# Kernel optimization log

Hardware: AMD Instinct MI355X
Metric: run time of the kernel (lower is better)

Reference implementation:

```python
import jax, jax.numpy as jnp
import numpy as np

N_HEADS = 4
D_HEAD = 32  # out_features // n_heads = 128 // 4
NEG_SLOPE = 0.2


def setup_inputs() -> dict:
    key = jax.random.key(0)
    k_x, k_adj, k_w, k_a = jax.random.split(key, 4)
    B, N, F_in, F_out = 4, 2048, 128, 128
    x = jax.random.normal(k_x, (B, N, F_in), dtype=jnp.float32)
    adj = jax.random.randint(k_adj, (B, N, N), 0, 2, dtype=jnp.int32)
    # Linear weight stored as [in, out] (torch stores [out, in]; math identical: x @ W)
    w_scale = np.sqrt(2.0 / (F_in + F_out))  # xavier-ish
    W = jax.random.normal(k_w, (F_in, F_out), dtype=jnp.float32) * w_scale
    a = jax.random.normal(k_a, (N_HEADS, 2 * D_HEAD), dtype=jnp.float32) * np.sqrt(2.0 / (2 * D_HEAD))
    return {"x": x, "adj": adj, "W": W, "a": a}


def reference(x, adj, W, a):
    B, N, _ = x.shape
    # project and split heads: [B, H, N, D]
    h = jnp.einsum('bnf,fo->bno', x, W).reshape(B, N, N_HEADS, D_HEAD).transpose(0, 2, 1, 3)
    # additive attention logits
    e_src = jnp.einsum('bhnd,hd->bhn', h, a[:, :D_HEAD])  # [B,H,N]
    e_dst = jnp.einsum('bhnd,hd->bhn', h, a[:, D_HEAD:])  # [B,H,N]
    e = e_src[:, :, :, None] + e_dst[:, :, None, :]       # [B,H,N,N]
    e = jnp.where(e > 0, e, NEG_SLOPE * e)                # leaky_relu(0.2)
    mask = (adj[:, None, :, :] == 0)                      # [B,1,N,N] -> broadcast over heads
    e = jnp.where(mask, -jnp.inf, e)
    alpha = jax.nn.softmax(e, axis=-1)                    # dropout omitted (eval mode)
    out = jnp.einsum('bhnm,bhmd->bhnd', alpha, h)         # weighted aggregation
    out = out.transpose(0, 2, 1, 3).reshape(B, N, N_HEADS * D_HEAD)
    return jax.nn.elu(out)
```

## Files before the change

kernel.cpp:

```cpp
#include <hip/hip_runtime.h>
#include <hip/hip_bf16.h>

#define BB 4
#define NN 2048
#define FIN 128
#define NH 4
#define DH 32
#define NS 0.2f

typedef unsigned int u32;
typedef unsigned short u16;
typedef unsigned long long u64;
typedef __attribute__((ext_vector_type(8))) short short8;
typedef __attribute__((ext_vector_type(4))) float f32x4;
typedef __attribute__((ext_vector_type(4))) unsigned int u32x4;

#define OFF_ES   0
#define OFF_PQ   32768
#define OFF_HT   65536
#define OFF_BITS 589824

__device__ __forceinline__ u16 f2bf_rne(float f) {
  unsigned u = __float_as_uint(f);
  return (u16)((u + 0x7fffu + ((u >> 16) & 1u)) >> 16);
}

__device__ __forceinline__ int bitmask(u32 w, int e) {
#if __has_builtin(__builtin_amdgcn_sbfe)
  return __builtin_amdgcn_sbfe((int)w, e, 1);
#else
  return ((int)(w << (31 - e))) >> 31;
#endif
}

__global__ __launch_bounds__(256) void k_pack(const int* __restrict__ adj,
                                              u32* __restrict__ bitsT) {
  __shared__ u32 tile[64][4];
  const int row0 = blockIdx.x * 4;
  const int wv = threadIdx.x >> 6;
  const int lane = threadIdx.x & 63;
  const int b = row0 >> 11, n0 = row0 & (NN - 1);
  const int* src = adj + (size_t)(row0 + wv) * NN;
#pragma unroll 8
  for (int it = 0; it < 32; ++it) {
    const u64 m = __ballot(src[it * 64 + lane] != 0);
    if (lane == 0) {
      tile[2 * it][wv] = (u32)m;
      tile[2 * it + 1][wv] = (u32)(m >> 32);
    }
  }
  __syncthreads();
  const int word = threadIdx.x >> 2, r = threadIdx.x & 3;
  bitsT[(size_t)b * 64 * NN + (size_t)word * NN + n0 + r] = tile[word][r];
}

__global__ __launch_bounds__(256) void k_proj(
    const float* __restrict__ x, const float* __restrict__ W,
    const float* __restrict__ a, u16* __restrict__ hT,
    float* __restrict__ e_src, u32* __restrict__ PQ) {
  __shared__ float Ws[FIN * 128];
  const int tid = threadIdx.x;
  const int f = tid & 127, g = tid >> 7;
  const float4* Wg4 = (const float4*)W;
  float4* Ws4 = (float4*)Ws;
#pragma unroll
  for (int t = 0; t < 16; ++t) Ws4[t * 256 + tid] = Wg4[t * 256 + tid];
  __syncthreads();

  const int rb = blockIdx.x * 16 + g * 8;
  const int head = f >> 5, d = f & 31;
  const int b = rb >> 11, n0 = rb & (NN - 1);
  const int bh = b * NH + head;
  const float a_s = a[head * (2 * DH) + d];
  const float a_d = a[head * (2 * DH) + DH + d];

  float acc[8];
#pragma unroll
  for (int r = 0; r < 8; ++r) acc[r] = 0.f;

  const float* xb = x + (size_t)rb * FIN;
  for (int k = 0; k < FIN; ++k) {
    const float wv = Ws[k * 128 + f];
#pragma unroll
    for (int r = 0; r < 8; ++r) acc[r] = fmaf(wv, xb[r * FIN + k], acc[r]);
  }

  u16 hs[8];
#pragma unroll
  for (int r = 0; r < 8; ++r) hs[r] = f2bf_rne(acc[r]);
  u16* dst = hT + ((size_t)bh * DH + d) * NN + n0;
  *(int4*)dst = *(int4*)&hs[0];

#pragma unroll
  for (int r = 0; r < 8; ++r) {
    float s1 = acc[r] * a_s;
    float s2 = acc[r] * a_d;
#pragma unroll
    for (int off = 16; off >= 1; off >>= 1) {
      s1 += __shfl_xor(s1, off);
      s2 += __shfl_xor(s2, off);
    }
    if (d == 0) {
      e_src[(size_t)bh * NN + n0 + r] = s1;
      const u32 pb = f2bf_rne(__expf(s2));
      const u32 qb = f2bf_rne(__expf(NS * s2));
      PQ[(size_t)bh * NN + n0 + r] = (qb << 16) | pb;
    }
  }
}

__global__ __launch_bounds__(256, 2) void k_attn(
    const u16* __restrict__ hT, const float* __restrict__ e_src,
    const u32* __restrict__ PQv, const u32* __restrict__ bitsT,
    float* __restrict__ out) {
  __shared__ float part[4][64][33];
  __shared__ float sp[4][4][16];

  const int bid = blockIdx.x;
  const int bh = bid >> 5;
  const int it = bid & 31;
  const int b = bh >> 2, head = bh & 3;

  const int w = threadIdx.x >> 6;
  const int lane = threadIdx.x & 63;
  const int lg = lane >> 4, lm = lane & 15;

  float A[4], B[4];
#pragma unroll
  for (int rs = 0; rs < 4; ++rs) {
    const float es = e_src[(size_t)bh * NN + it * 64 + rs * 16 + lm];
    A[rs] = __expf(es);
    B[rs] = __expf(NS * es);
  }

  const int jwbase = w * 512;
  const u32* PQb = PQv + (size_t)bh * NN + jwbase;
  const u16* hb0 = hT + ((size_t)bh * DH + lm) * NN + jwbase;
  const u16* hb1 = hT + ((size_t)bh * DH + 16 + lm) * NN + jwbase;
  const u32* btb = bitsT + (size_t)b * 64 * NN + (size_t)(w * 16) * NN + it * 64 + lm;
  const int shamt = lg * 8;
  const int jb = lg * 8;

  short8 ones;
#pragma unroll
  for (int e = 0; e < 8; ++e) ones[e] = (short)0x3F80;

  f32x4 acc00 = {0,0,0,0}, acc01 = {0,0,0,0};
  f32x4 acc10 = {0,0,0,0}, acc11 = {0,0,0,0};
  f32x4 acc20 = {0,0,0,0}, acc21 = {0,0,0,0};
  f32x4 acc30 = {0,0,0,0}, acc31 = {0,0,0,0};
  f32x4 accS0 = {0,0,0,0}, accS1 = {0,0,0,0};
  f32x4 accS2 = {0,0,0,0}, accS3 = {0,0,0,0};

#pragma unroll 4
  for (int t = 0; t < 16; ++t) {
    const int jj = t * 32 + jb;
    const u32x4 pqa = *(const u32x4*)(PQb + jj);
    const u32x4 pqb = *(const u32x4*)(PQb + jj + 4);
    const short8 hv0 = *(const short8*)(hb0 + jj);
    const short8 hv1 = *(const short8*)(hb1 + jj);
    const u32* btw = btb + (size_t)t * NN;
    const u32 wsh0 = btw[0] >> shamt;
    const u32 wsh1 = btw[16] >> shamt;
    const u32 wsh2 = btw[32] >> shamt;
    const u32 wsh3 = btw[48] >> shamt;
    short8 af0, af1, af2, af3;
#pragma unroll
    for (int e = 0; e < 8; ++e) {
      const u32 pq = (e < 4) ? pqa[e] : pqb[e - 4];
      const float Pf = __uint_as_float(pq << 16);
      const float Qf = __uint_as_float(pq & 0xffff0000u);
      const int m0 = bitmask(wsh0, e);
      const int m1 = bitmask(wsh1, e);
      const int m2 = bitmask(wsh2, e);
      const int m3 = bitmask(wsh3, e);
      float w0 = fmaxf(A[0] * Pf, B[0] * Qf);
      float w1 = fmaxf(A[1] * Pf, B[1] * Qf);
      float w2 = fmaxf(A[2] * Pf, B[2] * Qf);
      float w3 = fmaxf(A[3] * Pf, B[3] * Qf);
      w0 = __int_as_float(__float_as_int(w0) & m0);
      w1 = __int_as_float(__float_as_int(w1) & m1);
      w2 = __int_as_float(__float_as_int(w2) & m2);
      w3 = __int_as_float(__float_as_int(w3) & m3);
      af0[e] = (short)__builtin_bit_cast(unsigned short, __float2bfloat16(w0));
      af1[e] = (short)__builtin_bit_cast(unsigned short, __float2bfloat16(w1));
      af2[e] = (short)__builtin_bit_cast(unsigned short, __float2bfloat16(w2));
      af3[e] = (short)__builtin_bit_cast(unsigned short, __float2bfloat16(w3));
    }
    acc00 = __builtin_amdgcn_mfma_f32_16x16x32_bf16(af0, hv0, acc00, 0, 0, 0);
    acc01 = __builtin_amdgcn_mfma_f32_16x16x32_bf16(af0, hv1, acc01, 0, 0, 0);
    acc10 = __builtin_amdgcn_mfma_f32_16x16x32_bf16(af1, hv0, acc10, 0, 0, 0);
    acc11 = __builtin_amdgcn_mfma_f32_16x16x32_bf16(af1, hv1, acc11, 0, 0, 0);
    acc20 = __builtin_amdgcn_mfma_f32_16x16x32_bf16(af2, hv0, acc20, 0, 0, 0);
    acc21 = __builtin_amdgcn_mfma_f32_16x16x32_bf16(af2, hv1, acc21, 0, 0, 0);
    acc30 = __builtin_amdgcn_mfma_f32_16x16x32_bf16(af3, hv0, acc30, 0, 0, 0);
    acc31 = __builtin_amdgcn_mfma_f32_16x16x32_bf16(af3, hv1, acc31, 0, 0, 0);
    accS0 = __builtin_amdgcn_mfma_f32_16x16x32_bf16(af0, ones, accS0, 0, 0, 0);
    accS1 = __builtin_amdgcn_mfma_f32_16x16x32_bf16(af1, ones, accS1, 0, 0, 0);
    accS2 = __builtin_amdgcn_mfma_f32_16x16x32_bf16(af2, ones, accS2, 0, 0, 0);
    accS3 = __builtin_amdgcn_mfma_f32_16x16x32_bf16(af3, ones, accS3, 0, 0, 0);
  }

#pragma unroll
  for (int r = 0; r < 4; ++r) {
    const int rl = lg * 4 + r;
    part[w][rl][lm]           = acc00[r];
    part[w][rl][16 + lm]      = acc01[r];
    part[w][16 + rl][lm]      = acc10[r];
    part[w][16 + rl][16 + lm] = acc11[r];
    part[w][32 + rl][lm]      = acc20[r];
    part[w][32 + rl][16 + lm] = acc21[r];
    part[w][48 + rl][lm]      = acc30[r];
    part[w][48 + rl][16 + lm] = acc31[r];
  }
  if (lm == 0) {
#pragma unroll
    for (int r = 0; r < 4; ++r) {
      sp[w][0][lg * 4 + r] = accS0[r];
      sp[w][1][lg * 4 + r] = accS1[r];
      sp[w][2][lg * 4 + r] = accS2[r];
      sp[w][3][lg * 4 + r] = accS3[r];
    }
  }
  __syncthreads();

  const int tid = threadIdx.x;
#pragma unroll
  for (int t = 0; t < 8; ++t) {
    const int idx = t * 256 + tid;
    const int row = idx >> 5, d = idx & 31;
    const float v = part[0][row][d] + part[1][row][d] +
                    part[2][row][d] + part[3][row][d];
    const float s = sp[0][row >> 4][row & 15] + sp[1][row >> 4][row & 15] +
                    sp[2][row >> 4][row & 15] + sp[3][row >> 4][row & 15];
    const float o = v / s;
    const int n = it * 64 + row;
    out[((size_t)b * NN + n) * 128 + head * 32 + d] =
        o > 0.f ? o : (__expf(o) - 1.f);
  }
}

extern "C" void kernel_launch(void* const* d_in, const int* in_sizes, int n_in,
                              void* d_out, int out_size, void* d_ws, size_t ws_size,
                              hipStream_t stream) {
  const float* x = (const float*)d_in[0];
  const int* adj = (const int*)d_in[1];
  const float* W = (const float*)d_in[2];
  const float* a = (const float*)d_in[3];
  float* out = (float*)d_out;
  float* ws = (float*)d_ws;

  float* e_src = ws + OFF_ES;
  u32* PQv = (u32*)(ws + OFF_PQ);
  u16* hT = (u16*)(ws + OFF_HT);
  u32* bitsT = (u32*)(ws + OFF_BITS);

  k_pack<<<(BB * NN) / 4, 256, 0, stream>>>(adj, bitsT);
  k_proj<<<(BB * NN) / 16, 256, 0, stream>>>(x, W, a, hT, e_src, PQv);
  k_attn<<<BB * NH * 32, 256, 0, stream>>>(hT, e_src, PQv, bitsT, out);
}
```

Before: 63.91 us.

## Software-pipeline global loads in attention loop with inline asm and explicit vmcnt waits

Replaces the compiler-scheduled inner loop with a manual 4-slot ring of register buffers filled by inline-asm global loads issued two iterations ahead. Explicit s_waitcnt vmcnt barriers gate each compute step, so memory latency for the PQ, h and adjacency-bit loads overlaps with the bf16 conversion and MFMA work. This raises register pressure and ties correctness to exact load counts per stage. Because the loads are opaque asm, the compiler can no longer reorder them.

New measurement: 59.40 us, median of 3. 7.0% less time.

```diff
diff --git a/kernel.cpp b/kernel.cpp
--- a/kernel.cpp
+++ b/kernel.cpp
@@ -31,6 +31,21 @@
 #else
   return ((int)(w << (31 - e))) >> 31;
 #endif
+}
+
+template<int N> __device__ __forceinline__ void vmwait() {
+  asm volatile("s_waitcnt vmcnt(%0)" :: "n"(N) : "memory");
+  __builtin_amdgcn_sched_barrier(0);
+}
+__device__ __forceinline__ u32x4 gld4(const void* p) {
+  u32x4 r;
+  asm volatile("global_load_dwordx4 %0, %1, off" : "=v"(r) : "v"(p));
+  return r;
+}
+__device__ __forceinline__ u32 gld1(const void* p) {
+  u32 r;
+  asm volatile("global_load_dword %0, %1, off" : "=v"(r) : "v"(p));
+  return r;
 }
 
 __global__ __launch_bounds__(256) void k_pack(const int* __restrict__ adj,
@@ -152,54 +167,80 @@
   f32x4 accS0 = {0,0,0,0}, accS1 = {0,0,0,0};
   f32x4 accS2 = {0,0,0,0}, accS3 = {0,0,0,0};
 
-#pragma unroll 4
-  for (int t = 0; t < 16; ++t) {
-    const int jj = t * 32 + jb;
-    const u32x4 pqa = *(const u32x4*)(PQb + jj);
-    const u32x4 pqb = *(const u32x4*)(PQb + jj + 4);
-    const short8 hv0 = *(const short8*)(hb0 + jj);
-    const short8 hv1 = *(const short8*)(hb1 + jj);
-    const u32* btw = btb + (size_t)t * NN;
-    const u32 wsh0 = btw[0] >> shamt;
-    const u32 wsh1 = btw[16] >> shamt;
-    const u32 wsh2 = btw[32] >> shamt;
-    const u32 wsh3 = btw[48] >> shamt;
-    short8 af0, af1, af2, af3;
-#pragma unroll
-    for (int e = 0; e < 8; ++e) {
-      const u32 pq = (e < 4) ? pqa[e] : pqb[e - 4];
-      const float Pf = __uint_as_float(pq << 16);
-      const float Qf = __uint_as_float(pq & 0xffff0000u);
-      const int m0 = bitmask(wsh0, e);
-      const int m1 = bitmask(wsh1, e);
-      const int m2 = bitmask(wsh2, e);
-      const int m3 = bitmask(wsh3, e);
-      float w0 = fmaxf(A[0] * Pf, B[0] * Qf);
-      float w1 = fmaxf(A[1] * Pf, B[1] * Qf);
-      float w2 = fmaxf(A[2] * Pf, B[2] * Qf);
-      float w3 = fmaxf(A[3] * Pf, B[3] * Qf);
-      w0 = __int_as_float(__float_as_int(w0) & m0);
-      w1 = __int_as_float(__float_as_int(w1) & m1);
-      w2 = __int_as_float(__float_as_int(w2) & m2);
-      w3 = __int_as_float(__float_as_int(w3) & m3);
-      af0[e] = (short)__builtin_bit_cast(unsigned short, __float2bfloat16(w0));
-      af1[e] = (short)__builtin_bit_cast(unsigned short, __float2bfloat16(w1));
-      af2[e] = (short)__builtin_bit_cast(unsigned short, __float2bfloat16(w2));
-      af3[e] = (short)__builtin_bit_cast(unsigned short, __float2bfloat16(w3));
-    }
-    acc00 = __builtin_amdgcn_mfma_f32_16x16x32_bf16(af0, hv0, acc00, 0, 0, 0);
-    acc01 = __builtin_amdgcn_mfma_f32_16x16x32_bf16(af0, hv1, acc01, 0, 0, 0);
-    acc10 = __builtin_amdgcn_mfma_f32_16x16x32_bf16(af1, hv0, acc10, 0, 0, 0);
-    acc11 = __builtin_amdgcn_mfma_f32_16x16x32_bf16(af1, hv1, acc11, 0, 0, 0);
-    acc20 = __builtin_amdgcn_mfma_f32_16x16x32_bf16(af2, hv0, acc20, 0, 0, 0);
-    acc21 = __builtin_amdgcn_mfma_f32_16x16x32_bf16(af2, hv1, acc21, 0, 0, 0);
-    acc30 = __builtin_amdgcn_mfma_f32_16x16x32_bf16(af3, hv0, acc30, 0, 0, 0);
-    acc31 = __builtin_amdgcn_mfma_f32_16x16x32_bf16(af3, hv1, acc31, 0, 0, 0);
-    accS0 = __builtin_amdgcn_mfma_f32_16x16x32_bf16(af0, ones, accS0, 0, 0, 0);
-    accS1 = __builtin_amdgcn_mfma_f32_16x16x32_bf16(af1, ones, accS1, 0, 0, 0);
-    accS2 = __builtin_amdgcn_mfma_f32_16x16x32_bf16(af2, ones, accS2, 0, 0, 0);
-    accS3 = __builtin_amdgcn_mfma_f32_16x16x32_bf16(af3, ones, accS3, 0, 0, 0);
-  }
+  u32x4 pqa_[4], pqb_[4], h0_[4], h1_[4];
+  u32 b0_[4], b1_[4], b2_[4], b3_[4];
+
+#define ISSUE(tt, s) do { \
+    const int jjI = (tt) * 32 + jb; \
+    pqa_[s] = gld4(PQb + jjI); \
+    pqb_[s] = gld4(PQb + jjI + 4); \
+    h0_[s]  = gld4(hb0 + jjI); \
+    h1_[s]  = gld4(hb1 + jjI); \
+    const u32* bw_ = btb + (size_t)(tt) * NN; \
+    b0_[s] = gld1(bw_); \
+    b1_[s] = gld1(bw_ + 16); \
+    b2_[s] = gld1(bw_ + 32); \
+    b3_[s] = gld1(bw_ + 48); \
+  } while (0)
+
+#define COMPUTE(s) do { \
+    const u32x4 pqa = pqa_[s]; \
+    const u32x4 pqb = pqb_[s]; \
+    const short8 hv0 = __builtin_bit_cast(short8, h0_[s]); \
+    const short8 hv1 = __builtin_bit_cast(short8, h1_[s]); \
+    const u32 wsh0 = b0_[s] >> shamt; \
+    const u32 wsh1 = b1_[s] >> shamt; \
+    const u32 wsh2 = b2_[s] >> shamt; \
+    const u32 wsh3 = b3_[s] >> shamt; \
+    short8 af0, af1, af2, af3; \
+    _Pragma("unroll") \
+    for (int e = 0; e < 8; ++e) { \
+      const u32 pq = (e < 4) ? pqa[e] : pqb[e - 4]; \
+      const float Pf = __uint_as_float(pq << 16); \
+      const float Qf = __uint_as_float(pq & 0xffff0000u); \
+      float w0 = fmaxf(A[0] * Pf, B[0] * Qf); \
+      float w1 = fmaxf(A[1] * Pf, B[1] * Qf); \
+      float w2 = fmaxf(A[2] * Pf, B[2] * Qf); \
+      float w3 = fmaxf(A[3] * Pf, B[3] * Qf); \
+      w0 = __int_as_float(__float_as_int(w0) & bitmask(wsh0, e)); \
+      w1 = __int_as_float(__float_as_int(w1) & bitmask(wsh1, e)); \
+      w2 = __int_as_float(__float_as_int(w2) & bitmask(wsh2, e)); \
+      w3 = __int_as_float(__float_as_int(w3) & bitmask(wsh3, e)); \
+      af0[e] = (short)__builtin_bit_cast(unsigned short, __float2bfloat16(w0)); \
+      af1[e] = (short)__builtin_bit_cast(unsigned short, __float2bfloat16(w1)); \
+      af2[e] = (short)__builtin_bit_cast(unsigned short, __float2bfloat16(w2)); \
+      af3[e] = (short)__builtin_bit_cast(unsigned short, __float2bfloat16(w3)); \
+    } \
+    acc00 = __builtin_amdgcn_mfma_f32_16x16x32_bf16(af0, hv0, acc00, 0, 0, 0); \
+    acc01 = __builtin_amdgcn_mfma_f32_16x16x32_bf16(af0, hv1, acc01, 0, 0, 0); \
+    acc10 = __builtin_amdgcn_mfma_f32_16x16x32_bf16(af1, hv0, acc10, 0, 0, 0); \
+    acc11 = __builtin_amdgcn_mfma_f32_16x16x32_bf16(af1, hv1, acc11, 0, 0, 0); \
+    acc20 = __builtin_amdgcn_mfma_f32_16x16x32_bf16(af2, hv0, acc20, 0, 0, 0); \
+    acc21 = __builtin_amdgcn_mfma_f32_16x16x32_bf16(af2, hv1, acc21, 0, 0, 0); \
+    acc30 = __builtin_amdgcn_mfma_f32_16x16x32_bf16(af3, hv0, acc30, 0, 0, 0); \
+    acc31 = __builtin_amdgcn_mfma_f32_16x16x32_bf16(af3, hv1, acc31, 0, 0, 0); \
+    accS0 = __builtin_amdgcn_mfma_f32_16x16x32_bf16(af0, ones, accS0, 0, 0, 0); \
+    accS1 = __builtin_amdgcn_mfma_f32_16x16x32_bf16(af1, ones, accS1, 0, 0, 0); \
+    accS2 = __builtin_amdgcn_mfma_f32_16x16x32_bf16(af2, ones, accS2, 0, 0, 0); \
+    accS3 = __builtin_amdgcn_mfma_f32_16x16x32_bf16(af3, ones, accS3, 0, 0, 0); \
+  } while (0)
+
+  vmwait<0>();
+  ISSUE(0, 0);
+  ISSUE(1, 1);
+#pragma unroll
+  for (int t = 0; t < 12; ++t) {
+    ISSUE(t + 2, (t + 2) & 3);
+    vmwait<16>();
+    COMPUTE(t & 3);
+  }
+  ISSUE(14, 2); vmwait<16>(); COMPUTE(0);
+  ISSUE(15, 3); vmwait<16>(); COMPUTE(1);
+  vmwait<8>();  COMPUTE(2);
+  vmwait<0>();  COMPUTE(3);
+
+#undef ISSUE
+#undef COMPUTE
 
 #pragma unroll
   for (int r = 0; r < 4; ++r) {
```
